# Kernel tuning notes

Measured on AMD Instinct MI355X. Metric: run time of the kernel, lower is better.

Reference implementation:

```python
import jax, jax.numpy as jnp
import numpy as np

TAU = 0.2          # rank_temperature
LAM = 8.0          # lambda_value
TOPO = 0.5         # topology_influence
LEN_C = 0.01       # edge_length_coeff
SP_C = 0.001       # edge_sparsity_coeff
B, M, D = 4096, 256, 256


def _pairwise_sq(a, b):
    # [Na, D] x [Nb, D] -> [Na, Nb] squared L2 distances
    sq = (jnp.sum(a * a, -1)[:, None] - 2.0 * (a @ b.T)
          + jnp.sum(b * b, -1)[None, :])
    return jnp.maximum(sq, 0.0)


def setup_inputs() -> dict:
    key = jax.random.key(0)
    k1, k2, k3 = jax.random.split(key, 3)
    data = jax.random.normal(k1, (B, D), dtype=jnp.float32)
    weights = jax.random.uniform(k2, (M, D), dtype=jnp.float32)
    # edge logits initialized near edge_init_logit (-2.0) with small noise
    edge_logits = -2.0 + 0.1 * jax.random.normal(k3, (M, M), dtype=jnp.float32)
    return {"data": data, "weights": weights, "edge_logits": edge_logits}


def reference(data, weights, edge_logits):
    m = weights.shape[0]
    eye = jnp.eye(m, dtype=data.dtype)

    # distances: [B, M], l2
    distances = jnp.sqrt(_pairwise_sq(data, weights))

    # soft rank: [B, M]; pairwise sigmoid with zeroed diagonal
    diff = (distances[:, :, None] - distances[:, None, :]) / TAU  # [B, M, M]
    prob_greater = jax.nn.sigmoid(diff) * (1.0 - eye)[None]
    soft_rank = 1.0 + jnp.sum(prob_greater, axis=-1)

    # exponential neighborhood weighting
    neighborhood = jnp.exp(-(soft_rank - 1.0) / LAM)

    # symmetric edge probabilities with zero diagonal
    logits = 0.5 * (edge_logits + edge_logits.T)
    edge_prob = jax.nn.sigmoid(logits) * (1.0 - eye)

    degree = jnp.sum(edge_prob, axis=1) / float(m - 1)
    neighborhood = neighborhood * (1.0 + TOPO * degree[None, :])

    data_term = jnp.mean(neighborhood * distances)

    proto_dist = _pairwise_sq(weights, weights)  # sq_l2
    weighted_len = jnp.sum(edge_prob * proto_dist) / (jnp.sum(edge_prob) + 1e-8)
    sparsity = jnp.mean(edge_prob)

    loss = data_term + LEN_C * weighted_len + SP_C * sparsity
    return loss
```

## Files before the change

### kernel.cpp

```cpp
#include <hip/hip_runtime.h>
#include <math.h>

#define B_N 4096
#define M_N 256
#define D_N 256
#define ROWS 4
#define GRID_GEMM (B_N / ROWS)
#define GRID_RANK B_N
#define NSLOT 64

constexpr float TAU_   = 0.2f;
constexpr float LAM_   = 8.0f;
constexpr float TOPO_  = 0.5f;
constexpr float LEN_C_ = 0.01f;
constexpr float SP_C_  = 0.001f;
constexpr float LOG2E_ = 1.44269504088896340736f;
constexpr float KSC    = LOG2E_ / TAU_;
constexpr float KL     = LOG2E_ / LAM_;
constexpr float C0_    = 133.0f;


__device__ __forceinline__ float wave_reduce_sum(float v) {
#pragma unroll
  for (int off = 1; off < 64; off <<= 1) v += __shfl_xor(v, off, 64);
  return v;
}

__global__ __launch_bounds__(256) void k_prep(const float* __restrict__ w,
                                              const float* __restrict__ E,
                                              float* __restrict__ ws) {
  int tid = threadIdx.x;
  if (blockIdx.x < M_N) {
    float* wT = ws + 8192;
    int j = blockIdx.x, d = tid;
    float v = w[j * D_N + d];
    wT[d * M_N + j] = v;
    float s = wave_reduce_sum(v * v);
    __shared__ float red[4];
    if ((d & 63) == 0) red[d >> 6] = s;
    if (j == 0) {
      if (d < 16) ws[d] = 0.0f;
      if (d < NSLOT) {
        ws[2048 + 16 * d] = 0.0f;
        ((unsigned*)ws)[4096 + 16 * d] = 0u;
      }
    }
    __syncthreads();
    if (d == 0) ws[512 + j] = red[0] + red[1] + red[2] + red[3];
  } else {
    int j = blockIdx.x - M_N;
    int k = tid;
    __shared__ __align__(16) float swj[D_N];
    __shared__ float redp[4], redw[4];
    swj[k] = w[j * D_N + k];
    __syncthreads();

    float l = 0.5f * (E[j * M_N + k] + E[k * M_N + j]);
    float p = __builtin_amdgcn_rcpf(1.0f + __builtin_amdgcn_exp2f(-l * LOG2E_));
    if (k == j) p = 0.0f;

    float pd = 0.0f;
    const float4* wr = (const float4*)(w + (size_t)k * D_N);
    const float4* sw = (const float4*)swj;
#pragma unroll 8
    for (int i = 0; i < D_N / 4; i++) {
      float4 a = wr[i], b = sw[i];
      float dx = a.x - b.x, dy = a.y - b.y, dz = a.z - b.z, dw = a.w - b.w;
      pd += dx * dx + dy * dy + dz * dz + dw * dw;
    }

    float sp  = wave_reduce_sum(p);
    float spd = wave_reduce_sum(p * pd);
    if ((k & 63) == 0) { redp[k >> 6] = sp; redw[k >> 6] = spd; }
    __syncthreads();
    if (k == 0) {
      float tp = redp[0] + redp[1] + redp[2] + redp[3];
      float tw = redw[0] + redw[1] + redw[2] + redw[3];
      ws[16 + j]   = tp * (1.0f / (float)(M_N - 1));
      ws[1024 + j] = tp;
      ws[1280 + j] = tw;
    }
  }
}

__global__ __launch_bounds__(256) void k_gemm(const float* __restrict__ data,
                                              float* __restrict__ ws) {
  const float* wT    = ws + 8192;
  const float* wnorm = ws + 512;
  float* distG = ws + 131072;

  __shared__ float rednrm[ROWS][4];
  __shared__ float snrm[ROWS];

  const int tid  = threadIdx.x;
  const int wv_  = tid >> 6;
  const int lane = tid & 63;
  const int b0   = blockIdx.x * ROWS;

  float np[ROWS];
#pragma unroll
  for (int r = 0; r < ROWS; r++) {
    float x = data[(size_t)(b0 + r) * D_N + tid];
    np[r] = x * x;
  }
#pragma unroll
  for (int r = 0; r < ROWS; r++) {
    float s = wave_reduce_sum(np[r]);
    if (lane == 0) rednrm[r][wv_] = s;
  }
  __syncthreads();
  if (tid < ROWS)
    snrm[tid] = rednrm[tid][0] + rednrm[tid][1] + rednrm[tid][2] + rednrm[tid][3];

  const float4* x0 = (const float4*)(data + (size_t)(b0 + 0) * D_N);
  const float4* x1 = (const float4*)(data + (size_t)(b0 + 1) * D_N);
  const float4* x2 = (const float4*)(data + (size_t)(b0 + 2) * D_N);
  const float4* x3 = (const float4*)(data + (size_t)(b0 + 3) * D_N);
  float a0 = 0.f, a1 = 0.f, a2 = 0.f, a3 = 0.f;
#pragma unroll 4
  for (int d4 = 0; d4 < D_N / 4; d4++) {
    float4 xa = x0[d4], xb = x1[d4], xc = x2[d4], xd = x3[d4];
    const float* p = wT + (size_t)(4 * d4) * M_N + tid;
    float w0 = p[0], w1 = p[M_N], w2 = p[2 * M_N], w3 = p[3 * M_N];
    a0 = fmaf(xa.x, w0, a0); a0 = fmaf(xa.y, w1, a0);
    a0 = fmaf(xa.z, w2, a0); a0 = fmaf(xa.w, w3, a0);
    a1 = fmaf(xb.x, w0, a1); a1 = fmaf(xb.y, w1, a1);
    a1 = fmaf(xb.z, w2, a1); a1 = fmaf(xb.w, w3, a1);
    a2 = fmaf(xc.x, w0, a2); a2 = fmaf(xc.y, w1, a2);
    a2 = fmaf(xc.z, w2, a2); a2 = fmaf(xc.w, w3, a2);
    a3 = fmaf(xd.x, w0, a3); a3 = fmaf(xd.y, w1, a3);
    a3 = fmaf(xd.z, w2, a3); a3 = fmaf(xd.w, w3, a3);
  }
  __syncthreads();

  float wn = wnorm[tid];
  float acc[ROWS] = {a0, a1, a2, a3};
#pragma unroll
  for (int r = 0; r < ROWS; r++) {
    float sq = snrm[r] - 2.0f * acc[r] + wn;
    distG[(size_t)(b0 + r) * M_N + tid] = sqrtf(fmaxf(sq, 0.0f));
  }
}

__global__ __launch_bounds__(256) void k_rank(float* __restrict__ ws,
                                              float* __restrict__ out) {
  const float* distG  = ws + 131072;
  const float* degree = ws + 16;
  float* S_slot  = ws + 2048;
  unsigned* cnt1 = (unsigned*)ws + 4096;
  unsigned* cnt2 = (unsigned*)ws + 4;

  __shared__ __align__(16) float ew[M_N];
  __shared__ float redf[4], redp[4], redw[4];
  __shared__ int isLast;

  const int tid  = threadIdx.x;
  const int wv_  = tid >> 6;
  const int lane = tid & 63;
  const int row  = blockIdx.x;

  float dist = distG[(size_t)row * M_N + tid];
  float sc   = dist * KSC;
  float e    = __builtin_amdgcn_exp2f(sc - C0_);
  float iv   = __builtin_amdgcn_exp2f(C0_ - sc);
  float iv2  = iv * iv;
  ew[tid] = e;
  __syncthreads();

  float s = 0.0f;
  const float4* e4p = (const float4*)ew;
#pragma unroll 8
  for (int k4 = 0; k4 < M_N / 4; k4++) {
    float4 e4 = e4p[k4];
    float es1 = e4.x + e4.y, ep1 = e4.x * e4.y;
    float es2 = e4.z + e4.w, ep2 = e4.z * e4.w;
    float t1 = iv * es1;
    s = fmaf(t1 + 2.0f, __builtin_amdgcn_rcpf(fmaf(iv2, ep1, t1 + 1.0f)), s);
    float t2 = iv * es2;
    s = fmaf(t2 + 2.0f, __builtin_amdgcn_rcpf(fmaf(iv2, ep2, t2 + 1.0f)), s);
  }

  float nb = __builtin_amdgcn_exp2f((0.5f - s) * KL);
  float tl = nb * dist * (1.0f + TOPO_ * degree[tid]);

  float bs = wave_reduce_sum(tl);
  if (lane == 0) redf[wv_] = bs;
  __syncthreads();
  if (tid == 0) {
    float tot = redf[0] + redf[1] + redf[2] + redf[3];
    int slot = row & (NSLOT - 1);
    float old = atomicAdd(&S_slot[16 * slot], tot);
    asm volatile("" : "+v"(old));
    int last = 0;
    unsigned t1 = atomicAdd(&cnt1[16 * slot], 1u);
    if (t1 == (unsigned)(B_N / NSLOT - 1)) {
      unsigned t2 = atomicAdd(cnt2, 1u);
      last = (t2 == (unsigned)(NSLOT - 1)) ? 1 : 0;
    }
    isLast = last;
  }
  __syncthreads();

  if (isLast) {
    float p  = ws[1024 + tid];
    float wd = ws[1280 + tid];
    float rp = wave_reduce_sum(p);
    float rw = wave_reduce_sum(wd);
    if (lane == 0) { redp[wv_] = rp; redw[wv_] = rw; }
    float sd = 0.0f;
    if (wv_ == 0) {
      float v = atomicAdd(&S_slot[16 * lane], 0.0f);
      sd = wave_reduce_sum(v);
    }
    __syncthreads();
    if (tid == 0) {
      float Sp   = redp[0] + redp[1] + redp[2] + redp[3];
      float Swpd = redw[0] + redw[1] + redw[2] + redw[3];
      float data_term = sd * (1.0f / ((float)B_N * (float)M_N));
      float wl = Swpd / (Sp + 1e-8f);
      float sparsity = Sp * (1.0f / ((float)M_N * (float)M_N));
      out[0] = data_term + LEN_C_ * wl + SP_C_ * sparsity;
    }
  }
}

extern "C" void kernel_launch(void* const* d_in, const int* in_sizes, int n_in,
                              void* d_out, int out_size, void* d_ws, size_t ws_size,
                              hipStream_t stream) {
  const float* data = (const float*)d_in[0];
  const float* w    = (const float*)d_in[1];
  const float* E    = (const float*)d_in[2];
  float* ws = (float*)d_ws;

  k_prep<<<2 * M_N, 256, 0, stream>>>(w, E, ws);
  k_gemm<<<GRID_GEMM, 256, 0, stream>>>(data, ws);
  k_rank<<<GRID_RANK, 256, 0, stream>>>(ws, (float*)d_out);
}
```

Measured before the change: 109.9 us.

## Fuse distance GEMM and soft-rank kernels, precompute pairwise sums and products once per block

```diff
diff --git a/kernel.cpp b/kernel.cpp
--- a/kernel.cpp
+++ b/kernel.cpp
@@ -5,9 +5,9 @@
 #define M_N 256
 #define D_N 256
 #define ROWS 4
-#define GRID_GEMM (B_N / ROWS)
-#define GRID_RANK B_N
+#define GRID_MAIN (B_N / ROWS)
 #define NSLOT 64
+#define BLK_PER_SLOT (GRID_MAIN / NSLOT)
 
 constexpr float TAU_   = 0.2f;
 constexpr float LAM_   = 8.0f;
@@ -83,29 +83,32 @@
   }
 }
 
-__global__ __launch_bounds__(256) void k_gemm(const float* __restrict__ data,
-                                              float* __restrict__ ws) {
-  const float* wT    = ws + 8192;
-  const float* wnorm = ws + 512;
-  float* distG = ws + 131072;
-
+__global__ __launch_bounds__(256) void k_main(const float* __restrict__ data,
+                                              float* __restrict__ ws,
+                                              float* __restrict__ out) {
+  const float* wT     = ws + 8192;
+  const float* wnorm  = ws + 512;
+  const float* degree = ws + 16;
+  float* S_slot  = ws + 2048;
+  unsigned* cnt1 = (unsigned*)ws + 4096;
+  unsigned* cnt2 = (unsigned*)ws + 4;
+
+  __shared__ __align__(16) float ew[ROWS][M_N];
+  __shared__ __align__(16) float ewp[ROWS][M_N];
   __shared__ float rednrm[ROWS][4];
   __shared__ float snrm[ROWS];
+  __shared__ float redf[4], redp[4], redw[4];
+  __shared__ int isLast;
 
   const int tid  = threadIdx.x;
   const int wv_  = tid >> 6;
   const int lane = tid & 63;
   const int b0   = blockIdx.x * ROWS;
 
-  float np[ROWS];
 #pragma unroll
   for (int r = 0; r < ROWS; r++) {
     float x = data[(size_t)(b0 + r) * D_N + tid];
-    np[r] = x * x;
-  }
-#pragma unroll
-  for (int r = 0; r < ROWS; r++) {
-    float s = wave_reduce_sum(np[r]);
+    float s = wave_reduce_sum(x * x);
     if (lane == 0) rednrm[r][wv_] = s;
   }
   __syncthreads();
@@ -135,65 +138,58 @@
 
   float wn = wnorm[tid];
   float acc[ROWS] = {a0, a1, a2, a3};
+  float dist[ROWS], iv[ROWS], iv2[ROWS];
 #pragma unroll
   for (int r = 0; r < ROWS; r++) {
     float sq = snrm[r] - 2.0f * acc[r] + wn;
-    distG[(size_t)(b0 + r) * M_N + tid] = sqrtf(fmaxf(sq, 0.0f));
-  }
-}
-
-__global__ __launch_bounds__(256) void k_rank(float* __restrict__ ws,
-                                              float* __restrict__ out) {
-  const float* distG  = ws + 131072;
-  const float* degree = ws + 16;
-  float* S_slot  = ws + 2048;
-  unsigned* cnt1 = (unsigned*)ws + 4096;
-  unsigned* cnt2 = (unsigned*)ws + 4;
-
-  __shared__ __align__(16) float ew[M_N];
-  __shared__ float redf[4], redp[4], redw[4];
-  __shared__ int isLast;
-
-  const int tid  = threadIdx.x;
-  const int wv_  = tid >> 6;
-  const int lane = tid & 63;
-  const int row  = blockIdx.x;
-
-  float dist = distG[(size_t)row * M_N + tid];
-  float sc   = dist * KSC;
-  float e    = __builtin_amdgcn_exp2f(sc - C0_);
-  float iv   = __builtin_amdgcn_exp2f(C0_ - sc);
-  float iv2  = iv * iv;
-  ew[tid] = e;
-  __syncthreads();
-
-  float s = 0.0f;
-  const float4* e4p = (const float4*)ew;
+    dist[r] = sqrtf(fmaxf(sq, 0.0f));
+    float sc = dist[r] * KSC;
+    ew[r][tid] = __builtin_amdgcn_exp2f(sc - C0_);
+    iv[r]      = __builtin_amdgcn_exp2f(C0_ - sc);
+    iv2[r]     = iv[r] * iv[r];
+  }
+  __syncthreads();
+
+#pragma unroll
+  for (int h = 0; h < 2; h++) {
+    int p  = tid + h * 256;
+    int r  = p >> 7, idx = p & 127;
+    float ea = ew[r][2 * idx], eb = ew[r][2 * idx + 1];
+    ewp[r][2 * idx]     = ea + eb;
+    ewp[r][2 * idx + 1] = ea * eb;
+  }
+  __syncthreads();
+
+  float fj = 1.0f + TOPO_ * degree[tid];
+  float tl = 0.0f;
+#pragma unroll
+  for (int r = 0; r < ROWS; r++) {
+    float s = 0.0f;
+    const float4* q4 = (const float4*)(&ewp[r][0]);
+    float ivr = iv[r], iv2r = iv2[r];
 #pragma unroll 8
-  for (int k4 = 0; k4 < M_N / 4; k4++) {
-    float4 e4 = e4p[k4];
-    float es1 = e4.x + e4.y, ep1 = e4.x * e4.y;
-    float es2 = e4.z + e4.w, ep2 = e4.z * e4.w;
-    float t1 = iv * es1;
-    s = fmaf(t1 + 2.0f, __builtin_amdgcn_rcpf(fmaf(iv2, ep1, t1 + 1.0f)), s);
-    float t2 = iv * es2;
-    s = fmaf(t2 + 2.0f, __builtin_amdgcn_rcpf(fmaf(iv2, ep2, t2 + 1.0f)), s);
-  }
-
-  float nb = __builtin_amdgcn_exp2f((0.5f - s) * KL);
-  float tl = nb * dist * (1.0f + TOPO_ * degree[tid]);
+    for (int k4 = 0; k4 < M_N / 4; k4++) {
+      float4 q = q4[k4];
+      float t1 = ivr * q.x;
+      s = fmaf(t1 + 2.0f, __builtin_amdgcn_rcpf(fmaf(iv2r, q.y, t1 + 1.0f)), s);
+      float t2 = ivr * q.z;
+      s = fmaf(t2 + 2.0f, __builtin_amdgcn_rcpf(fmaf(iv2r, q.w, t2 + 1.0f)), s);
+    }
+    float nb = __builtin_amdgcn_exp2f((0.5f - s) * KL);
+    tl = fmaf(nb * dist[r], fj, tl);
+  }
 
   float bs = wave_reduce_sum(tl);
   if (lane == 0) redf[wv_] = bs;
   __syncthreads();
   if (tid == 0) {
     float tot = redf[0] + redf[1] + redf[2] + redf[3];
-    int slot = row & (NSLOT - 1);
+    int slot = (int)(blockIdx.x & (NSLOT - 1));
     float old = atomicAdd(&S_slot[16 * slot], tot);
     asm volatile("" : "+v"(old));
     int last = 0;
     unsigned t1 = atomicAdd(&cnt1[16 * slot], 1u);
-    if (t1 == (unsigned)(B_N / NSLOT - 1)) {
+    if (t1 == (unsigned)(BLK_PER_SLOT - 1)) {
       unsigned t2 = atomicAdd(cnt2, 1u);
       last = (t2 == (unsigned)(NSLOT - 1)) ? 1 : 0;
     }
@@ -233,6 +229,5 @@
   float* ws = (float*)d_ws;
 
   k_prep<<<2 * M_N, 256, 0, stream>>>(w, E, ws);
-  k_gemm<<<GRID_GEMM, 256, 0, stream>>>(data, ws);
-  k_rank<<<GRID_RANK, 256, 0, stream>>>(ws, (float*)d_out);
-}
+  k_main<<<GRID_MAIN, 256, 0, stream>>>(data, ws, (float*)d_out);
+}
```

New measurement: 102.2 us. 7.0% less time.
